# Performance work log

Hardware: AMD Instinct MI355X
Metric: run time of the kernel (lower is better)

The kernel has to match this reference:

```python
import jax, jax.numpy as jnp
import numpy as np

N_NODES = 50000


def setup_inputs() -> dict:
    key = jax.random.key(0)
    k1, k2, k3, k4, k5, k6 = jax.random.split(key, 6)
    N, T, F_IN, F_OUT, E = N_NODES, 4, 64, 64, 800000
    node_features = jax.random.normal(k1, (N, T, F_IN), dtype=jnp.float32)
    edge_weights = jax.random.uniform(k2, (T, E), dtype=jnp.float32)
    src = jax.random.randint(k3, (E,), 0, N, dtype=jnp.int32)
    dst = jax.random.randint(k4, (E,), 0, N, dtype=jnp.int32)
    weight = jax.random.normal(k5, (F_OUT, F_IN), dtype=jnp.float32) / np.sqrt(F_IN)
    bias = jax.random.normal(k6, (F_OUT,), dtype=jnp.float32) * 0.01
    return {"node_features": node_features, "edge_weights": edge_weights,
            "src": src, "dst": dst, "weight": weight, "bias": bias}


def reference(node_features, edge_weights, src, dst, weight, bias):
    # edge_weights: (T, E) -> per-edge weights (E, T)
    ew = edge_weights.T  # (E, T)
    # gather source node features: (E, T, F); multiply by per-edge/timestep scalar
    msg = ew[:, :, None] * node_features[src]  # (E, T, F)
    # scatter-sum into destination nodes: (N, T, F)
    h = jax.ops.segment_sum(msg, dst, num_segments=N_NODES)
    # final linear: (N, T, F_out)
    out = jnp.einsum('ntf,of->nto', h, weight) + bias
    return out
```

## Files before the change

### kernel.cpp

```cpp
#include <hip/hip_runtime.h>


#define F_DIM 64
#define TF 256

__device__ __forceinline__ unsigned short f2bf(float x) {
  unsigned u = __float_as_uint(x);
  return (unsigned short)((u + 0x7FFF + ((u >> 16) & 1)) >> 16);
}
__device__ __forceinline__ float bf2f(unsigned short b) {
  return __uint_as_float(((unsigned)b) << 16);
}
__device__ __forceinline__ void fma4(float4& a, float s, float4 w) {
  a.x += s * w.x; a.y += s * w.y; a.z += s * w.z; a.w += s * w.w;
}

__global__ __launch_bounds__(1024) void scanA_kernel(
    const int* __restrict__ cnt, int* __restrict__ off, int* __restrict__ bsum, int N) {
  __shared__ int wsum[16];
  int tid = threadIdx.x;
  int i = blockIdx.x * 1024 + tid;
  int v = (i < N) ? cnt[i] : 0;
  int lane = tid & 63;
  int incl = v;
  #pragma unroll
  for (int s = 1; s < 64; s <<= 1) {
    int t = __shfl_up(incl, s, 64);
    if (lane >= s) incl += t;
  }
  int w = tid >> 6;
  if (lane == 63) wsum[w] = incl;
  __syncthreads();
  if (w == 0) {
    int x = (lane < 16) ? wsum[lane] : 0;
    #pragma unroll
    for (int s = 1; s < 16; s <<= 1) {
      int t = __shfl_up(x, s, 64);
      if (lane >= s) x += t;
    }
    if (lane < 16) wsum[lane] = x;
  }
  __syncthreads();
  int wpre = (w == 0) ? 0 : wsum[w - 1];
  if (i < N) off[i] = wpre + incl - v;
  if (tid == 1023) bsum[blockIdx.x] = wpre + incl;
}

__global__ __launch_bounds__(64) void scanB_kernel(int* __restrict__ bsum, int nb) {
  int lane = threadIdx.x;
  int v = (lane < nb) ? bsum[lane] : 0;
  int incl = v;
  #pragma unroll
  for (int s = 1; s < 64; s <<= 1) {
    int t = __shfl_up(incl, s, 64);
    if (lane >= s) incl += t;
  }
  if (lane < nb) bsum[lane] = incl - v;
}

__global__ __launch_bounds__(256) void fill_kernel(
    const int* __restrict__ dst, const int* __restrict__ src,
    const float* __restrict__ ew, const int* __restrict__ off,
    const int* __restrict__ bsum, int* __restrict__ cnt,
    uint4* __restrict__ rec, int E) {
  int e = blockIdx.x * 256 + threadIdx.x;
  if (e < E) {
    int d = dst[e];
    int pos = off[d] + bsum[d >> 10] + atomicSub(&cnt[d], 1) - 1;
    unsigned w0 = f2bf(ew[e]),         w1 = f2bf(ew[E + e]);
    unsigned w2 = f2bf(ew[2 * E + e]), w3 = f2bf(ew[3 * E + e]);
    uint4 r;
    r.x = (unsigned)src[e];
    r.y = (w1 << 16) | w0;
    r.z = (w3 << 16) | w2;
    r.w = 0;
    rec[pos] = r;
  }
}

__global__ __launch_bounds__(256) void transform_hist_kernel(
    const float4* __restrict__ nf4, const float* __restrict__ W,
    unsigned short* __restrict__ nfb, int nrows,
    const int* __restrict__ dst, int* __restrict__ cnt, int E, int epb) {
  __shared__ float Wt[64 * 64];
  __shared__ float rows[128][65];
  int tid = threadIdx.x;

  {
    int e0 = blockIdx.x * epb;
    int e1 = min(e0 + epb, E);
    for (int e = e0 + tid; e < e1; e += 256) atomicAdd(&cnt[dst[e]], 1);
  }

  #pragma unroll
  for (int i = tid; i < 4096; i += 256) Wt[(i & 63) * 64 + (i >> 6)] = W[i];
  int rbase = blockIdx.x * 128;
  if (rbase >= nrows) return;
  int nr = min(128, nrows - rbase);
  for (int i = tid; i < nr * 16; i += 256) {
    int r = i >> 4, q = i & 15;
    float4 v = nf4[(size_t)(rbase + r) * 16 + q];
    rows[r][q * 4 + 0] = v.x; rows[r][q * 4 + 1] = v.y;
    rows[r][q * 4 + 2] = v.z; rows[r][q * 4 + 3] = v.w;
  }
  __syncthreads();

  int oq = tid & 7;
  int r0 = (tid >> 3) * 4;
  float4 acc[4][2];
  #pragma unroll
  for (int j = 0; j < 4; ++j) {
    acc[j][0] = make_float4(0.f, 0.f, 0.f, 0.f);
    acc[j][1] = make_float4(0.f, 0.f, 0.f, 0.f);
  }
  const float4* Wt4 = (const float4*)Wt;
  #pragma unroll 8
  for (int f = 0; f < 64; ++f) {
    float4 w0 = Wt4[f * 16 + oq * 2 + 0];
    float4 w1 = Wt4[f * 16 + oq * 2 + 1];
    #pragma unroll
    for (int j = 0; j < 4; ++j) {
      float rv = rows[r0 + j][f];
      fma4(acc[j][0], rv, w0);
      fma4(acc[j][1], rv, w1);
    }
  }
  int obase = oq * 8;
  #pragma unroll
  for (int j = 0; j < 4; ++j) {
    if (r0 + j < nr) {
      size_t rowoff = (size_t)(rbase + r0 + j) * F_DIM + obase;
      #pragma unroll
      for (int c = 0; c < 2; ++c) {
        float4 a = acc[j][c];
        ushort4 u = make_ushort4(f2bf(a.x), f2bf(a.y), f2bf(a.z), f2bf(a.w));
        *reinterpret_cast<ushort4*>(&nfb[rowoff + c * 4]) = u;
      }
    }
  }
}

__global__ __launch_bounds__(256) void gather_bf16_kernel(
    const ushort4* __restrict__ nfb, const uint4* __restrict__ rec,
    const int* __restrict__ off, const int* __restrict__ bsum,
    const float4* __restrict__ bias4, float4* __restrict__ out4, int N, int E) {
  int idx = blockIdx.x * 256 + threadIdx.x;
  int n = idx >> 6;
  if (n >= N) return;
  n = __builtin_amdgcn_readfirstlane(n);
  int r = idx & 63, t = r >> 4, q = r & 15;
  int wsel = t >> 1;
  int wshift = (t & 1) << 4;
  int beg = off[n] + bsum[n >> 10];
  int end = (n + 1 < N) ? off[n + 1] + bsum[(n + 1) >> 10] : E;
  beg = __builtin_amdgcn_readfirstlane(beg);
  end = __builtin_amdgcn_readfirstlane(end);

  float4 acc = make_float4(0.f, 0.f, 0.f, 0.f);
  int p = beg;
  for (; p + 4 <= end; p += 4) {
    uint4 r0 = rec[p], r1 = rec[p + 1], r2 = rec[p + 2], r3 = rec[p + 3];
    float w0 = __uint_as_float(((wsel ? r0.z : r0.y) >> wshift) << 16);
    float w1 = __uint_as_float(((wsel ? r1.z : r1.y) >> wshift) << 16);
    float w2 = __uint_as_float(((wsel ? r2.z : r2.y) >> wshift) << 16);
    float w3 = __uint_as_float(((wsel ? r3.z : r3.y) >> wshift) << 16);
    ushort4 v0 = nfb[(size_t)r0.x * 64 + t * 16 + q];
    ushort4 v1 = nfb[(size_t)r1.x * 64 + t * 16 + q];
    ushort4 v2 = nfb[(size_t)r2.x * 64 + t * 16 + q];
    ushort4 v3 = nfb[(size_t)r3.x * 64 + t * 16 + q];
    acc.x += w0 * bf2f(v0.x) + w1 * bf2f(v1.x) + w2 * bf2f(v2.x) + w3 * bf2f(v3.x);
    acc.y += w0 * bf2f(v0.y) + w1 * bf2f(v1.y) + w2 * bf2f(v2.y) + w3 * bf2f(v3.y);
    acc.z += w0 * bf2f(v0.z) + w1 * bf2f(v1.z) + w2 * bf2f(v2.z) + w3 * bf2f(v3.z);
    acc.w += w0 * bf2f(v0.w) + w1 * bf2f(v1.w) + w2 * bf2f(v2.w) + w3 * bf2f(v3.w);
  }
  for (; p < end; ++p) {
    uint4 rr = rec[p];
    float w = __uint_as_float(((wsel ? rr.z : rr.y) >> wshift) << 16);
    ushort4 v = nfb[(size_t)rr.x * 64 + t * 16 + q];
    acc.x += w * bf2f(v.x); acc.y += w * bf2f(v.y);
    acc.z += w * bf2f(v.z); acc.w += w * bf2f(v.w);
  }
  float4 b = bias4[q];
  float4 res = make_float4(acc.x + b.x, acc.y + b.y, acc.z + b.z, acc.w + b.w);
  out4[(size_t)n * 64 + t * 16 + q] = res;
}

__global__ __launch_bounds__(256) void hist_kernel(
    const int* __restrict__ dst, int* __restrict__ cnt, int E) {
  int e = blockIdx.x * 256 + threadIdx.x;
  if (e < E) atomicAdd(&cnt[dst[e]], 1);
}

__global__ __launch_bounds__(256) void gather_f32_kernel(
    const float4* __restrict__ nf4, const uint4* __restrict__ rec,
    const int* __restrict__ off, const int* __restrict__ bsum,
    float4* __restrict__ h4, int N, int E) {
  int idx = blockIdx.x * 256 + threadIdx.x;
  int n = idx >> 6;
  if (n >= N) return;
  int r = idx & 63, t = r >> 4, q = r & 15;
  int wsel = t >> 1;
  int wshift = (t & 1) << 4;
  int beg = off[n] + bsum[n >> 10];
  int end = (n + 1 < N) ? off[n + 1] + bsum[(n + 1) >> 10] : E;
  float4 acc = make_float4(0.f, 0.f, 0.f, 0.f);
  for (int p = beg; p < end; ++p) {
    uint4 rr = rec[p];
    float w = __uint_as_float(((wsel ? rr.z : rr.y) >> wshift) << 16);
    float4 v = nf4[(size_t)rr.x * 64 + t * 16 + q];
    acc.x += w * v.x; acc.y += w * v.y; acc.z += w * v.z; acc.w += w * v.w;
  }
  h4[(size_t)n * 64 + t * 16 + q] = acc;
}

__global__ __launch_bounds__(256) void linear_kernel(
    float* __restrict__ h, const float* __restrict__ W,
    const float* __restrict__ bias, int nrows) {
  __shared__ float Wt[64 * 65];
  __shared__ float rows[4][64];
  int tid = threadIdx.x;
  for (int i = tid; i < 4096; i += 256) Wt[(i & 63) * 65 + (i >> 6)] = W[i];
  int rr = tid >> 6, o = tid & 63;
  float b = bias[o];
  int rbase = blockIdx.x * 32;
  for (int r0 = 0; r0 < 32; r0 += 4) {
    int row = rbase + r0 + rr;
    __syncthreads();
    if (row < nrows) rows[rr][o] = h[(size_t)row * F_DIM + o];
    __syncthreads();
    if (row < nrows) {
      float acc = b;
      #pragma unroll
      for (int f = 0; f < 64; ++f) acc += rows[rr][f] * Wt[f * 65 + o];
      h[(size_t)row * F_DIM + o] = acc;
    }
  }
}

extern "C" void kernel_launch(void* const* d_in, const int* in_sizes, int n_in,
                              void* d_out, int out_size, void* d_ws, size_t ws_size,
                              hipStream_t stream) {
  const float* nf   = (const float*)d_in[0];
  const float* ew   = (const float*)d_in[1];
  const int*   src  = (const int*)d_in[2];
  const int*   dst  = (const int*)d_in[3];
  const float* W    = (const float*)d_in[4];
  const float* bias = (const float*)d_in[5];
  float* out = (float*)d_out;

  int E = in_sizes[2];
  int N = out_size / TF;
  int nrows = out_size / F_DIM;
  int nfelems = nrows * F_DIM;

  char* wsb = (char*)d_ws;
  int* cnt  = (int*)wsb;
  int* off  = cnt + N;
  int* bsum = off + (N + 1);
  size_t ofs = ((size_t)(2 * N + 1 + 64) * 4 + 15) & ~(size_t)15;
  uint4* rec = (uint4*)(wsb + ofs);           ofs += (size_t)E * 16;
  ofs = (ofs + 511) & ~(size_t)511;
  unsigned short* nfb = (unsigned short*)(wsb + ofs);
  size_t need_bf16 = ofs + (size_t)nfelems * 2;
  bool use_bf16 = ws_size >= need_bf16;

  (void)hipMemsetAsync(cnt, 0, (size_t)N * sizeof(int), stream);

  int eblk = (E + 255) / 256;
  int sblk = (N + 1023) / 1024;

  if (use_bf16) {
    int tblocks = (nrows + 127) / 128;
    int epb = (E + tblocks - 1) / tblocks;
    transform_hist_kernel<<<tblocks, 256, 0, stream>>>(
        (const float4*)nf, W, nfb, nrows, dst, cnt, E, epb);
    scanA_kernel<<<sblk, 1024, 0, stream>>>(cnt, off, bsum, N);
    scanB_kernel<<<1, 64, 0, stream>>>(bsum, sblk);
    fill_kernel<<<eblk, 256, 0, stream>>>(dst, src, ew, off, bsum, cnt, rec, E);
    gather_bf16_kernel<<<(N * 64 + 255) / 256, 256, 0, stream>>>(
        (const ushort4*)nfb, rec, off, bsum, (const float4*)bias,
        (float4*)out, N, E);
  } else {
    hist_kernel<<<eblk, 256, 0, stream>>>(dst, cnt, E);
    scanA_kernel<<<sblk, 1024, 0, stream>>>(cnt, off, bsum, N);
    scanB_kernel<<<1, 64, 0, stream>>>(bsum, sblk);
    fill_kernel<<<eblk, 256, 0, stream>>>(dst, src, ew, off, bsum, cnt, rec, E);
    gather_f32_kernel<<<(N * 64 + 255) / 256, 256, 0, stream>>>(
        (const float4*)nf, rec, off, bsum, (float4*)out, N, E);
    linear_kernel<<<(nrows + 31) / 32, 256, 0, stream>>>(out, W, bias, nrows);
  }
}
```

Baseline: 176.7 us.

## Use bf16 MFMA for node-feature linear transform with grid-stride wave tiles

```diff
diff --git a/kernel.cpp b/kernel.cpp
--- a/kernel.cpp
+++ b/kernel.cpp
@@ -3,6 +3,10 @@
 
 #define F_DIM 64
 #define TF 256
+
+typedef __attribute__((ext_vector_type(8))) short bf16x8;
+typedef __attribute__((ext_vector_type(4))) float f32x4;
+union frag_u { bf16x8 v; unsigned short s[8]; };
 
 __device__ __forceinline__ unsigned short f2bf(float x) {
   unsigned u = __float_as_uint(x);
@@ -10,9 +14,6 @@
 }
 __device__ __forceinline__ float bf2f(unsigned short b) {
   return __uint_as_float(((unsigned)b) << 16);
-}
-__device__ __forceinline__ void fma4(float4& a, float s, float4 w) {
-  a.x += s * w.x; a.y += s * w.y; a.z += s * w.z; a.w += s * w.w;
 }
 
 __global__ __launch_bounds__(1024) void scanA_kernel(
@@ -81,63 +82,65 @@
 __global__ __launch_bounds__(256) void transform_hist_kernel(
     const float4* __restrict__ nf4, const float* __restrict__ W,
     unsigned short* __restrict__ nfb, int nrows,
-    const int* __restrict__ dst, int* __restrict__ cnt, int E, int epb) {
-  __shared__ float Wt[64 * 64];
-  __shared__ float rows[128][65];
-  int tid = threadIdx.x;
-
-  {
-    int e0 = blockIdx.x * epb;
-    int e1 = min(e0 + epb, E);
-    for (int e = e0 + tid; e < e1; e += 256) atomicAdd(&cnt[dst[e]], 1);
-  }
-
+    const int* __restrict__ dst, int* __restrict__ cnt, int E) {
+  int lane = threadIdx.x & 63;
+  int l15 = lane & 15, lg = lane >> 4;
+  int wid = (blockIdx.x * 256 + threadIdx.x) >> 6;
+  int nw = (gridDim.x * 256) >> 6;
+
+  frag_u a[4][2];
   #pragma unroll
-  for (int i = tid; i < 4096; i += 256) Wt[(i & 63) * 64 + (i >> 6)] = W[i];
-  int rbase = blockIdx.x * 128;
-  if (rbase >= nrows) return;
-  int nr = min(128, nrows - rbase);
-  for (int i = tid; i < nr * 16; i += 256) {
-    int r = i >> 4, q = i & 15;
-    float4 v = nf4[(size_t)(rbase + r) * 16 + q];
-    rows[r][q * 4 + 0] = v.x; rows[r][q * 4 + 1] = v.y;
-    rows[r][q * 4 + 2] = v.z; rows[r][q * 4 + 3] = v.w;
-  }
-  __syncthreads();
-
-  int oq = tid & 7;
-  int r0 = (tid >> 3) * 4;
-  float4 acc[4][2];
-  #pragma unroll
-  for (int j = 0; j < 4; ++j) {
-    acc[j][0] = make_float4(0.f, 0.f, 0.f, 0.f);
-    acc[j][1] = make_float4(0.f, 0.f, 0.f, 0.f);
-  }
-  const float4* Wt4 = (const float4*)Wt;
-  #pragma unroll 8
-  for (int f = 0; f < 64; ++f) {
-    float4 w0 = Wt4[f * 16 + oq * 2 + 0];
-    float4 w1 = Wt4[f * 16 + oq * 2 + 1];
+  for (int ot = 0; ot < 4; ++ot) {
     #pragma unroll
-    for (int j = 0; j < 4; ++j) {
-      float rv = rows[r0 + j][f];
-      fma4(acc[j][0], rv, w0);
-      fma4(acc[j][1], rv, w1);
-    }
-  }
-  int obase = oq * 8;
-  #pragma unroll
-  for (int j = 0; j < 4; ++j) {
-    if (r0 + j < nr) {
-      size_t rowoff = (size_t)(rbase + r0 + j) * F_DIM + obase;
+    for (int kh = 0; kh < 2; ++kh) {
+      const float* wp = W + (ot * 16 + l15) * 64 + kh * 32 + lg * 8;
+      float4 v0 = *reinterpret_cast<const float4*>(wp);
+      float4 v1 = *reinterpret_cast<const float4*>(wp + 4);
+      a[ot][kh].s[0] = f2bf(v0.x); a[ot][kh].s[1] = f2bf(v0.y);
+      a[ot][kh].s[2] = f2bf(v0.z); a[ot][kh].s[3] = f2bf(v0.w);
+      a[ot][kh].s[4] = f2bf(v1.x); a[ot][kh].s[5] = f2bf(v1.y);
+      a[ot][kh].s[6] = f2bf(v1.z); a[ot][kh].s[7] = f2bf(v1.w);
+    }
+  }
+
+  int ntiles = (nrows + 15) >> 4;
+  for (int tile = wid; tile < ntiles; tile += nw) {
+    int r = tile * 16 + l15;
+    int rc = min(r, nrows - 1);
+    const float4* bp = nf4 + (size_t)rc * 16 + lg * 2;
+    float4 v0 = bp[0], v1 = bp[1];
+    float4 v2 = bp[8], v3 = bp[9];
+    frag_u b0, b1;
+    b0.s[0] = f2bf(v0.x); b0.s[1] = f2bf(v0.y);
+    b0.s[2] = f2bf(v0.z); b0.s[3] = f2bf(v0.w);
+    b0.s[4] = f2bf(v1.x); b0.s[5] = f2bf(v1.y);
+    b0.s[6] = f2bf(v1.z); b0.s[7] = f2bf(v1.w);
+    b1.s[0] = f2bf(v2.x); b1.s[1] = f2bf(v2.y);
+    b1.s[2] = f2bf(v2.z); b1.s[3] = f2bf(v2.w);
+    b1.s[4] = f2bf(v3.x); b1.s[5] = f2bf(v3.y);
+    b1.s[6] = f2bf(v3.z); b1.s[7] = f2bf(v3.w);
+
+    f32x4 acc[4];
+    #pragma unroll
+    for (int ot = 0; ot < 4; ++ot) {
+      f32x4 z = {0.f, 0.f, 0.f, 0.f};
+      acc[ot] = __builtin_amdgcn_mfma_f32_16x16x32_bf16(a[ot][0].v, b0.v, z, 0, 0, 0);
+      acc[ot] = __builtin_amdgcn_mfma_f32_16x16x32_bf16(a[ot][1].v, b1.v, acc[ot], 0, 0, 0);
+    }
+    if (r < nrows) {
       #pragma unroll
-      for (int c = 0; c < 2; ++c) {
-        float4 a = acc[j][c];
-        ushort4 u = make_ushort4(f2bf(a.x), f2bf(a.y), f2bf(a.z), f2bf(a.w));
-        *reinterpret_cast<ushort4*>(&nfb[rowoff + c * 4]) = u;
+      for (int ot = 0; ot < 4; ++ot) {
+        ushort4 u = make_ushort4(f2bf(acc[ot][0]), f2bf(acc[ot][1]),
+                                 f2bf(acc[ot][2]), f2bf(acc[ot][3]));
+        *reinterpret_cast<ushort4*>(
+            &nfb[(size_t)r * F_DIM + ot * 16 + lg * 4]) = u;
       }
     }
   }
+
+  int gtid = blockIdx.x * 256 + threadIdx.x;
+  int gsz = gridDim.x * 256;
+  for (int e = gtid; e < E; e += gsz) atomicAdd(&cnt[dst[e]], 1);
 }
 
 __global__ __launch_bounds__(256) void gather_bf16_kernel(
@@ -270,10 +273,8 @@
   int sblk = (N + 1023) / 1024;
 
   if (use_bf16) {
-    int tblocks = (nrows + 127) / 128;
-    int epb = (E + tblocks - 1) / tblocks;
-    transform_hist_kernel<<<tblocks, 256, 0, stream>>>(
-        (const float4*)nf, W, nfb, nrows, dst, cnt, E, epb);
+    transform_hist_kernel<<<1024, 256, 0, stream>>>(
+        (const float4*)nf, W, nfb, nrows, dst, cnt, E);
     scanA_kernel<<<sblk, 1024, 0, stream>>>(cnt, off, bsum, N);
     scanB_kernel<<<1, 64, 0, stream>>>(bsum, sblk);
     fill_kernel<<<eblk, 256, 0, stream>>>(dst, src, ew, off, bsum, cnt, rec, E);
```

Result: faster. 160.2 us (-9.3%).
